# Kernel optimization log

Hardware: AMD Instinct MI355X
Metric: run time of the kernel (lower is better)

Reference implementation:

```python
import jax, jax.numpy as jnp
import numpy as np

NB_TS = 4          # module-level global nb_timestep in the original code
EMBED = 512
SQRT_DIM = float(np.sqrt(EMBED))


def _conv(x, w, b=None):
    # torch Conv2d(kernel=3, stride=1, padding=1), NCHW / OIHW
    y = jax.lax.conv_general_dilated(x, w, (1, 1), ((1, 1), (1, 1)),
                                     dimension_numbers=('NCHW', 'OIHW', 'NCHW'))
    if b is not None:
        y = y + b[None, :, None, None]
    return y


def setup_inputs() -> dict:
    B, C, H, W = 8, 512, 16, 16
    TXT = 256
    key = jax.random.key(0)
    ks = iter(jax.random.split(key, 40))

    def nrm(shape, s=0.02):
        return jax.random.normal(next(ks), shape, jnp.float32) * s

    inp = {
        'x':   jax.random.normal(next(ks), (B, C, H, W), jnp.float32),
        'txt': jax.random.normal(next(ks), (B, 1, TXT), jnp.float32),
        # attention convs
        'Wa_w': nrm((C, C, 3, 3)), 'Wa_b': nrm((C,)),
        'Ua_w': nrm((C, C, 3, 3)), 'Ua_b': nrm((C,)),
        'Va_w': nrm((1, C, 3, 3)),
        # gate convs
        'Wi_w': nrm((C, C, 3, 3)), 'Wi_b': nrm((C,)),
        'Ui_w': nrm((C, C, 3, 3)), 'Ui_b': nrm((C,)),
        'Wf_w': nrm((C, C, 3, 3)), 'Wf_b': nrm((C,)),
        'Uf_w': nrm((C, C, 3, 3)), 'Uf_b': nrm((C,)),
        'Wc_w': nrm((C, C, 3, 3)), 'Wc_b': nrm((C,)),
        'Uc_w': nrm((C, C, 3, 3)), 'Uc_b': nrm((C,)),
        'Wo_w': nrm((C, C, 3, 3)), 'Wo_b': nrm((C,)),
        'Uo_w': nrm((C, C, 3, 3)), 'Uo_b': nrm((C,)),
        # text attention linears (torch Linear weight layout [out, in])
        'WQ': nrm((EMBED * H * W, TXT)),
        'WK': nrm((EMBED, 1)),
        'WV': nrm((EMBED, 1)),
        'Wsum_w': nrm((1, EMBED)), 'Wsum_b': nrm((1,)),
    }
    return inp


def reference(x, txt, Wa_w, Wa_b, Ua_w, Ua_b, Va_w,
              Wi_w, Wi_b, Ui_w, Ui_b, Wf_w, Wf_b, Uf_w, Uf_b,
              Wc_w, Wc_b, Uc_w, Uc_b, Wo_w, Wo_b, Uo_w, Uo_b,
              WQ, WK, WV, Wsum_w, Wsum_b):
    B, _, Hs, Ws = x.shape
    txt2 = txt.reshape(txt.shape[0], txt.shape[2])  # [B, 256]
    h = x
    c = x
    # Q is timestep-invariant; hoist out of the loop (same math)
    Q = (txt2 @ WQ.T).reshape(B, Hs, Ws, EMBED)  # [B,H,W,E]
    for _ in range(NB_TS):
        Z = _conv(jnp.tanh(_conv(h, Wa_w, Wa_b) + _conv(x, Ua_w, Ua_b)), Va_w)  # [B,1,H,W]
        A1 = jax.nn.softmax(Z, axis=1)          # softmax over channel dim of size 1 (faithful)
        Ap = jnp.transpose(A1, (0, 2, 3, 1))    # [B,H,W,1]
        K = Ap @ WK.T                            # [B,H,W,E]
        V = Ap @ WV.T                            # [B,H,W,E]
        scores = jnp.sum(Q * K, axis=3, keepdims=True) / SQRT_DIM  # [B,H,W,1]
        attn = jax.nn.softmax(scores, axis=1)    # torch softmax(dim=1) -> over H axis
        # repeat(...,embed_dim)*V is just a broadcast multiply
        A2 = (attn * V) @ Wsum_w.T + Wsum_b      # [B,H,W,1]
        A2 = jnp.transpose(A2, (0, 3, 1, 2))     # [B,1,H,W]
        myA = A1 + A2
        AM = myA * x
        i = jax.nn.sigmoid(_conv(AM, Wi_w, Wi_b) + _conv(h, Ui_w, Ui_b))
        f = jax.nn.sigmoid(_conv(AM, Wf_w, Wf_b) + _conv(h, Uf_w, Uf_b))
        o = jax.nn.sigmoid(_conv(AM, Wo_w, Wo_b) + _conv(h, Uo_w, Uo_b))
        g = jnp.tanh(_conv(AM, Wc_w, Wc_b) + _conv(h, Uc_w, Uc_b))
        c = g * i + f * c
        h = jnp.tanh(c) * o
    return h
```

## Files before the change

### kernel.cpp

```cpp
#include <hip/hip_runtime.h>

typedef unsigned short u16;
typedef __attribute__((ext_vector_type(8))) _Float16 f16x8;
typedef __attribute__((ext_vector_type(4))) float f32x4;
typedef __attribute__((ext_vector_type(4))) int i32x4;
typedef __attribute__((ext_vector_type(4))) unsigned short us4;

__device__ __forceinline__ u16 f2h(float f) {
  _Float16 h = (_Float16)f;
  return __builtin_bit_cast(unsigned short, h);
}
__device__ __forceinline__ float sigm(float v) { return 1.0f / (1.0f + __expf(-v)); }
__device__ __forceinline__ float tanh_(float v) {
  float t = __expf(-2.0f * fabsf(v));
  float r = (1.0f - t) / (1.0f + t);
  return v >= 0.0f ? r : -r;
}

typedef const __attribute__((address_space(1))) unsigned int* gas_t;
typedef __attribute__((address_space(3))) unsigned int* las_t;
__device__ __forceinline__ void gl16(const u16* g, u16* l) {
  __builtin_amdgcn_global_load_lds((gas_t)g, (las_t)l, 16, 0, 0);
}

__global__ void prep_big(const float* __restrict__ WQ, const float* __restrict__ WK,
                         const float* __restrict__ txt, const float* __restrict__ WV,
                         const float* __restrict__ Wsw, const float* __restrict__ Wsb,
                         const float* __restrict__ wi, const float* __restrict__ wf,
                         const float* __restrict__ wo, const float* __restrict__ wc,
                         const float* __restrict__ ui, const float* __restrict__ uf,
                         const float* __restrict__ uo, const float* __restrict__ uc,
                         u16* __restrict__ dstW, u16* __restrict__ dstU,
                         float* __restrict__ scores, float* __restrict__ sb) {
  __shared__ float wk[512];
  __shared__ float red[4];
  int tid = threadIdx.x;
  if (blockIdx.x < 256) {
    int lane = tid & 63, wave = tid >> 6;
    wk[tid] = WK[tid];
    wk[tid + 256] = WK[tid + 256];
    __syncthreads();
    size_t p = blockIdx.x;
    const float* base = WQ + p * 131072 + tid;
    float m = 0.f;
#pragma unroll 8
    for (int e = 0; e < 512; ++e) m = fmaf(base[(size_t)e * 256], wk[e], m);
    for (int b = 0; b < 8; ++b) {
      float v = m * txt[b * 256 + tid];
#pragma unroll
      for (int off = 32; off > 0; off >>= 1) v += __shfl_down(v, off, 64);
      if (lane == 0) red[wave] = v;
      __syncthreads();
      if (tid == 0)
        scores[b * 256 + p] = (red[0] + red[1] + red[2] + red[3]) * 0.044194173824159216f;
      __syncthreads();
    }
    if (blockIdx.x == 0) {
      float v = WV[tid] * Wsw[tid] + WV[tid + 256] * Wsw[tid + 256];
#pragma unroll
      for (int off = 32; off > 0; off >>= 1) v += __shfl_down(v, off, 64);
      if (lane == 0) red[wave] = v;
      __syncthreads();
      if (tid == 0) {
        sb[0] = red[0] + red[1] + red[2] + red[3];
        sb[1] = Wsb[0];
      }
    }
    return;
  }
  int idx = (blockIdx.x - 256) * 256 + tid;
  const int PERSET = 4718592;
  int set = idx >= PERSET ? 1 : 0;
  int o = idx - set * PERSET;
  int j = o * 2;
  int ci = j & 31;
  int gch = (j >> 5) & 63;
  int t = j >> 11;
  int k9 = t % 9;
  int cc = t / 9;
  int chunk = cc & 15, chgrp = cc >> 4;
  int gate = gch >> 4, chrow = gch & 15;
  int ch = chgrp * 16 + chrow;
  int cin = chunk * 32 + ci;
  const float* s;
  if (set == 0) s = gate == 0 ? wi : gate == 1 ? wf : gate == 2 ? wo : wc;
  else          s = gate == 0 ? ui : gate == 1 ? uf : gate == 2 ? uo : uc;
  size_t si = (size_t)(ch * 512 + cin) * 9 + k9;
  unsigned int lo = f2h(s[si]);
  unsigned int hi = f2h(s[si + 9]);
  unsigned int* d = (unsigned int*)(set == 0 ? dstW : dstU);
  d[o] = lo | (hi << 16);
}

__global__ void prep_inputs(const float* __restrict__ x, const float* __restrict__ scores,
                            const float* __restrict__ sb,
                            u16* __restrict__ AM, u16* __restrict__ H0) {
  int idx = blockIdx.x * 256 + threadIdx.x;
  int ch = idx & 511, p = (idx >> 9) & 255, b = idx >> 17;
  int w = p & 15, h = p >> 4;
  float s = sb[0], b0 = sb[1];
  float mx = -1e30f;
#pragma unroll
  for (int hh = 0; hh < 16; ++hh) mx = fmaxf(mx, scores[b * 256 + hh * 16 + w]);
  float den = 0.f, my = 0.f;
#pragma unroll
  for (int hh = 0; hh < 16; ++hh) {
    float e = __expf(scores[b * 256 + hh * 16 + w] - mx);
    den += e;
    if (hh == h) my = e;
  }
  float coef = 1.0f + b0 + s * my / den;
  float xv = x[(size_t)(b * 512 + ch) * 256 + p];
  AM[idx] = f2h(coef * xv);
  H0[idx] = f2h(xv);
}

template <int MODE>
__launch_bounds__(256, 1)
__global__ void conv4(const u16* __restrict__ inA, const u16* __restrict__ inH,
                      const u16* __restrict__ wW, const u16* __restrict__ wU,
                      const float* __restrict__ bWi, const float* __restrict__ bUi,
                      const float* __restrict__ bWf, const float* __restrict__ bUf,
                      const float* __restrict__ bWo, const float* __restrict__ bUo,
                      const float* __restrict__ bWc, const float* __restrict__ bUc,
                      float* __restrict__ G, const float* __restrict__ c_src,
                      float* __restrict__ c_dst, u16* __restrict__ h_out,
                      float* __restrict__ out) {
  __shared__ __align__(16) u16 Alds[2][9 * 64 * 32];
  __shared__ __align__(16) u16 Blds[2][18 * 18 * 32];
  const int tid = threadIdx.x;
  const int b = blockIdx.x >> 5, chgrp = blockIdx.x & 31;
  const int wave = tid >> 6, lane = tid & 63;
  const int row = lane & 15, quad = lane >> 4;
  const int NCH = (MODE == 0) ? 32 : 16;

  {
    i32x4 z = {0, 0, 0, 0};
    i32x4* bz = (i32x4*)Blds;
#pragma unroll
    for (int i = 0; i < 11; ++i) {
      int k = tid + 256 * i;
      if (k < 2592) bz[k] = z;
    }
  }

  const u16* wsrcW = (MODE == 0) ? wW + (size_t)chgrp * 294912 : nullptr;
  const u16* wsrcU = wU + (size_t)chgrp * 294912;
  const u16* isrcA = (MODE == 0) ? inA + (size_t)b * 131072 : nullptr;
  const u16* isrcH = inH + (size_t)b * 131072;

  auto stage = [&](int k, int buf) {
    const u16* gw;
    const u16* gi;
    if (MODE == 0 && k < 16) { gw = wsrcW + k * 18432; gi = isrcA + (k & 15) * 32; }
    else                     { gw = wsrcU + (k & 15) * 18432; gi = isrcH + (k & 15) * 32; }
#pragma unroll
    for (int i = 0; i < 9; ++i)
      gl16(gw + (size_t)(i * 256 + tid) * 8, &Alds[buf][(i * 256 + (tid & 192)) * 8]);
#pragma unroll
    for (int j = 0; j < 4; ++j) {
      int y = j * 4 + wave;
      gl16(gi + (size_t)(y * 16 + (lane >> 2)) * 512 + (lane & 3) * 8,
           &Blds[buf][(y + 1) * 576 + 32]);
    }
  };

  f32x4 acc[4][4];
#pragma unroll
  for (int m = 0; m < 4; ++m)
#pragma unroll
    for (int n = 0; n < 4; ++n) acc[m][n] = (f32x4){0.f, 0.f, 0.f, 0.f};

  const int ch0 = chgrp * 16 + quad * 4;
  float* gptr = G + (((size_t)blockIdx.x * 4 + wave) * 16) * 256 + lane * 4;

  stage(0, 0);
  __syncthreads();

#pragma unroll 2
  for (int k = 0; k < NCH; ++k) {
    int cur = k & 1;
    if (k + 1 < NCH) stage(k + 1, cur ^ 1);
    const u16* A = Alds[cur];
    const u16* B = Blds[cur];
#pragma unroll
    for (int kx = 0; kx < 3; ++kx) {
      f16x8 bfr[6];
#pragma unroll
      for (int jj = 0; jj < 6; ++jj)
        bfr[jj] = *(const f16x8*)(&B[(wave * 4 + jj) * 576 + (row + kx) * 32 + quad * 8]);
#pragma unroll
      for (int ky = 0; ky < 3; ++ky) {
#pragma unroll
        for (int m = 0; m < 4; ++m) {
          f16x8 af = *(const f16x8*)(&A[((ky * 3 + kx) * 64 + m * 16 + row) * 32 + quad * 8]);
#pragma unroll
          for (int n = 0; n < 4; ++n)
            acc[m][n] = __builtin_amdgcn_mfma_f32_16x16x32_f16(af, bfr[n + ky], acc[m][n], 0, 0, 0);
        }
      }
    }
    if constexpr (MODE == 0) {
      if (k == 15) {
#pragma unroll
        for (int m = 0; m < 4; ++m) {
          const float* bw = m == 0 ? bWi : m == 1 ? bWf : m == 2 ? bWo : bWc;
          const float* bu = m == 0 ? bUi : m == 1 ? bUf : m == 2 ? bUo : bUc;
          f32x4 bias;
#pragma unroll
          for (int r = 0; r < 4; ++r) bias[r] = bw[ch0 + r] + bu[ch0 + r];
#pragma unroll
          for (int n = 0; n < 4; ++n) {
            acc[m][n] = acc[m][n] + bias;
            *(f32x4*)(gptr + (m * 4 + n) * 256) = acc[m][n];
          }
        }
      }
    }
    __syncthreads();
  }

#pragma unroll
  for (int n = 0; n < 4; ++n) {
    const int p = (wave * 4 + n) * 16 + row;
    f32x4 zi = acc[0][n], zf = acc[1][n], zo = acc[2][n], zg = acc[3][n];
    if constexpr (MODE != 0) {
      zi = zi + *(const f32x4*)(gptr + (0 + n) * 256);
      zf = zf + *(const f32x4*)(gptr + (4 + n) * 256);
      zo = zo + *(const f32x4*)(gptr + (8 + n) * 256);
      zg = zg + *(const f32x4*)(gptr + (12 + n) * 256);
    }
    f32x4 cold;
#pragma unroll
    for (int r = 0; r < 4; ++r)
      cold[r] = c_src[(size_t)(b * 512 + ch0 + r) * 256 + p];
    f32x4 cnew, hv;
#pragma unroll
    for (int r = 0; r < 4; ++r) {
      float iv = sigm(zi[r]);
      float fv = sigm(zf[r]);
      float ov = sigm(zo[r]);
      float gv = tanh_(zg[r]);
      float cn = fmaf(gv, iv, fv * cold[r]);
      cnew[r] = cn;
      hv[r] = tanh_(cn) * ov;
    }
    if constexpr (MODE != 2) {
#pragma unroll
      for (int r = 0; r < 4; ++r)
        c_dst[(size_t)(b * 512 + ch0 + r) * 256 + p] = cnew[r];
      us4 hb;
      hb[0] = f2h(hv[0]); hb[1] = f2h(hv[1]);
      hb[2] = f2h(hv[2]); hb[3] = f2h(hv[3]);
      *(us4*)(h_out + (size_t)b * 131072 + (size_t)p * 512 + ch0) = hb;
    } else {
#pragma unroll
      for (int r = 0; r < 4; ++r)
        out[(size_t)(b * 512 + ch0 + r) * 256 + p] = hv[r];
    }
  }
}

extern "C" void kernel_launch(void* const* d_in, const int* in_sizes, int n_in,
                              void* d_out, int out_size, void* d_ws, size_t ws_size,
                              hipStream_t stream) {
  const float* x    = (const float*)d_in[0];
  const float* txt  = (const float*)d_in[1];
  const float* Wi_w = (const float*)d_in[7];
  const float* Wi_b = (const float*)d_in[8];
  const float* Ui_w = (const float*)d_in[9];
  const float* Ui_b = (const float*)d_in[10];
  const float* Wf_w = (const float*)d_in[11];
  const float* Wf_b = (const float*)d_in[12];
  const float* Uf_w = (const float*)d_in[13];
  const float* Uf_b = (const float*)d_in[14];
  const float* Wc_w = (const float*)d_in[15];
  const float* Wc_b = (const float*)d_in[16];
  const float* Uc_w = (const float*)d_in[17];
  const float* Uc_b = (const float*)d_in[18];
  const float* Wo_w = (const float*)d_in[19];
  const float* Wo_b = (const float*)d_in[20];
  const float* Uo_w = (const float*)d_in[21];
  const float* Uo_b = (const float*)d_in[22];
  const float* WQ   = (const float*)d_in[23];
  const float* WK   = (const float*)d_in[24];
  const float* WV   = (const float*)d_in[25];
  const float* Wsw  = (const float*)d_in[26];
  const float* Wsb  = (const float*)d_in[27];
  (void)in_sizes; (void)n_in; (void)ws_size;

  char* ws = (char*)d_ws;
  size_t off = 0;
  auto carve = [&](size_t n) {
    char* p = ws + off;
    off += (n + 255) & ~(size_t)255;
    return p;
  };
  u16* WswzW    = (u16*)carve(18874368);
  u16* WswzU    = (u16*)carve(18874368);
  u16* AM       = (u16*)carve(2097152);
  u16* H0       = (u16*)carve(2097152);
  u16* H1       = (u16*)carve(2097152);
  float* G      = (float*)carve(16777216);
  float* C      = (float*)carve(4194304);
  float* scores = (float*)carve(8192);
  float* sb     = (float*)carve(256);

  prep_big<<<37120, 256, 0, stream>>>(WQ, WK, txt, WV, Wsw, Wsb,
                                      Wi_w, Wf_w, Wo_w, Wc_w,
                                      Ui_w, Uf_w, Uo_w, Uc_w,
                                      WswzW, WswzU, scores, sb);
  prep_inputs<<<4096, 256, 0, stream>>>(x, scores, sb, AM, H0);

  conv4<0><<<256, 256, 0, stream>>>(AM, H0, WswzW, WswzU,
                                    Wi_b, Ui_b, Wf_b, Uf_b, Wo_b, Uo_b, Wc_b, Uc_b,
                                    G, x, C, H1, nullptr);
  conv4<1><<<256, 256, 0, stream>>>(nullptr, H1, nullptr, WswzU,
                                    nullptr, nullptr, nullptr, nullptr,
                                    nullptr, nullptr, nullptr, nullptr,
                                    G, C, C, H0, nullptr);
  conv4<1><<<256, 256, 0, stream>>>(nullptr, H0, nullptr, WswzU,
                                    nullptr, nullptr, nullptr, nullptr,
                                    nullptr, nullptr, nullptr, nullptr,
                                    G, C, C, H1, nullptr);
  conv4<2><<<256, 256, 0, stream>>>(nullptr, H1, nullptr, WswzU,
                                    nullptr, nullptr, nullptr, nullptr,
                                    nullptr, nullptr, nullptr, nullptr,
                                    G, C, nullptr, nullptr, (float*)d_out);
}
```

Measured before the change: 555.8 us.

## Split conv blocks by spatial half, single-buffer LDS, restructure prep kernels

The score GEMV is split over 8 embedding slices, with partial results combined by atomicAdd into a zeroed buffer. The weight swizzle now stages each strip through LDS and writes it out with coalesced 16-byte stores. The conv kernels split each batch image into two row halves, which doubles the grid to 512 blocks and allows 2 blocks per CU. In exchange they drop LDS double buffering and use explicit sync-stage-sync, so loads no longer overlap compute within a block. Weights are also loaded twice as often in total, since each half refetches them.

```diff
diff --git a/kernel.cpp b/kernel.cpp
--- a/kernel.cpp
+++ b/kernel.cpp
@@ -32,33 +32,35 @@
                          const float* __restrict__ uo, const float* __restrict__ uc,
                          u16* __restrict__ dstW, u16* __restrict__ dstU,
                          float* __restrict__ scores, float* __restrict__ sb) {
-  __shared__ float wk[512];
+  __shared__ __align__(16) u16 L[9 * 64 * 32];
+  __shared__ float wk[64];
   __shared__ float red[4];
   int tid = threadIdx.x;
-  if (blockIdx.x < 256) {
-    int lane = tid & 63, wave = tid >> 6;
-    wk[tid] = WK[tid];
-    wk[tid + 256] = WK[tid + 256];
+  if (blockIdx.x < 2048) {
+    int p = blockIdx.x & 255;
+    int es = blockIdx.x >> 8;
+    if (tid < 64) wk[tid] = WK[es * 64 + tid];
     __syncthreads();
-    size_t p = blockIdx.x;
-    const float* base = WQ + p * 131072 + tid;
+    const float* base = WQ + (size_t)p * 131072 + (size_t)es * 16384 + tid;
     float m = 0.f;
 #pragma unroll 8
-    for (int e = 0; e < 512; ++e) m = fmaf(base[(size_t)e * 256], wk[e], m);
+    for (int e = 0; e < 64; ++e) m = fmaf(base[(size_t)e * 256], wk[e], m);
+    int lane = tid & 63, wave = tid >> 6;
     for (int b = 0; b < 8; ++b) {
       float v = m * txt[b * 256 + tid];
 #pragma unroll
-      for (int off = 32; off > 0; off >>= 1) v += __shfl_down(v, off, 64);
+      for (int off = 32; off; off >>= 1) v += __shfl_down(v, off, 64);
       if (lane == 0) red[wave] = v;
       __syncthreads();
       if (tid == 0)
-        scores[b * 256 + p] = (red[0] + red[1] + red[2] + red[3]) * 0.044194173824159216f;
+        atomicAdd(&scores[b * 256 + p],
+                  (red[0] + red[1] + red[2] + red[3]) * 0.044194173824159216f);
       __syncthreads();
     }
     if (blockIdx.x == 0) {
       float v = WV[tid] * Wsw[tid] + WV[tid + 256] * Wsw[tid + 256];
 #pragma unroll
-      for (int off = 32; off > 0; off >>= 1) v += __shfl_down(v, off, 64);
+      for (int off = 32; off; off >>= 1) v += __shfl_down(v, off, 64);
       if (lane == 0) red[wave] = v;
       __syncthreads();
       if (tid == 0) {
@@ -68,28 +70,30 @@
     }
     return;
   }
-  int idx = (blockIdx.x - 256) * 256 + tid;
-  const int PERSET = 4718592;
-  int set = idx >= PERSET ? 1 : 0;
-  int o = idx - set * PERSET;
-  int j = o * 2;
-  int ci = j & 31;
-  int gch = (j >> 5) & 63;
-  int t = j >> 11;
-  int k9 = t % 9;
-  int cc = t / 9;
-  int chunk = cc & 15, chgrp = cc >> 4;
+  int sbid = blockIdx.x - 2048;
+  int set = sbid >> 9;
+  int chgrp = (sbid >> 4) & 31;
+  int chunk = sbid & 15;
+  int q = tid & 3, gch = tid >> 2;
   int gate = gch >> 4, chrow = gch & 15;
   int ch = chgrp * 16 + chrow;
-  int cin = chunk * 32 + ci;
   const float* s;
   if (set == 0) s = gate == 0 ? wi : gate == 1 ? wf : gate == 2 ? wo : wc;
   else          s = gate == 0 ? ui : gate == 1 ? uf : gate == 2 ? uo : uc;
-  size_t si = (size_t)(ch * 512 + cin) * 9 + k9;
-  unsigned int lo = f2h(s[si]);
-  unsigned int hi = f2h(s[si + 9]);
-  unsigned int* d = (unsigned int*)(set == 0 ? dstW : dstU);
-  d[o] = lo | (hi << 16);
+  const float* strip = s + (size_t)(ch * 512 + chunk * 32) * 9;
+#pragma unroll
+  for (int c8 = 0; c8 < 8; ++c8) {
+    int cl = q * 8 + c8;
+#pragma unroll
+    for (int k9 = 0; k9 < 9; ++k9)
+      L[(k9 * 64 + gch) * 32 + cl] = f2h(strip[cl * 9 + k9]);
+  }
+  __syncthreads();
+  u16* dst = (set == 0 ? dstW : dstU) + (size_t)(chgrp * 16 + chunk) * 18432;
+  i32x4* d4 = (i32x4*)dst;
+  i32x4* l4 = (i32x4*)L;
+#pragma unroll
+  for (int i = 0; i < 9; ++i) d4[i * 256 + tid] = l4[i * 256 + tid];
 }
 
 __global__ void prep_inputs(const float* __restrict__ x, const float* __restrict__ scores,
@@ -116,7 +120,7 @@
 }
 
 template <int MODE>
-__launch_bounds__(256, 1)
+__launch_bounds__(256, 2)
 __global__ void conv4(const u16* __restrict__ inA, const u16* __restrict__ inH,
                       const u16* __restrict__ wW, const u16* __restrict__ wU,
                       const float* __restrict__ bWi, const float* __restrict__ bUi,
@@ -126,76 +130,78 @@
                       float* __restrict__ G, const float* __restrict__ c_src,
                       float* __restrict__ c_dst, u16* __restrict__ h_out,
                       float* __restrict__ out) {
-  __shared__ __align__(16) u16 Alds[2][9 * 64 * 32];
-  __shared__ __align__(16) u16 Blds[2][18 * 18 * 32];
+  __shared__ __align__(16) u16 Alds[9 * 64 * 32];
+  __shared__ __align__(16) u16 Blds[10 * 18 * 32];
   const int tid = threadIdx.x;
-  const int b = blockIdx.x >> 5, chgrp = blockIdx.x & 31;
+  const int chgrp = blockIdx.x & 31;
+  const int nhalf = (blockIdx.x >> 5) & 1;
+  const int b = blockIdx.x >> 6;
   const int wave = tid >> 6, lane = tid & 63;
   const int row = lane & 15, quad = lane >> 4;
   const int NCH = (MODE == 0) ? 32 : 16;
+  const int gyBase = nhalf * 8 - 1;
 
   {
     i32x4 z = {0, 0, 0, 0};
     i32x4* bz = (i32x4*)Blds;
 #pragma unroll
-    for (int i = 0; i < 11; ++i) {
+    for (int i = 0; i < 6; ++i) {
       int k = tid + 256 * i;
-      if (k < 2592) bz[k] = z;
-    }
-  }
-
-  const u16* wsrcW = (MODE == 0) ? wW + (size_t)chgrp * 294912 : nullptr;
+      if (k < 1440) bz[k] = z;
+    }
+  }
+  __syncthreads();
+
+  const u16* wsrcW = wW + (size_t)chgrp * 294912;
   const u16* wsrcU = wU + (size_t)chgrp * 294912;
-  const u16* isrcA = (MODE == 0) ? inA + (size_t)b * 131072 : nullptr;
+  const u16* isrcA = inA + (size_t)b * 131072;
   const u16* isrcH = inH + (size_t)b * 131072;
 
-  auto stage = [&](int k, int buf) {
+  auto stage = [&](int k) {
     const u16* gw;
     const u16* gi;
-    if (MODE == 0 && k < 16) { gw = wsrcW + k * 18432; gi = isrcA + (k & 15) * 32; }
+    if (MODE == 0 && k < 16) { gw = wsrcW + k * 18432; gi = isrcA + k * 32; }
     else                     { gw = wsrcU + (k & 15) * 18432; gi = isrcH + (k & 15) * 32; }
 #pragma unroll
     for (int i = 0; i < 9; ++i)
-      gl16(gw + (size_t)(i * 256 + tid) * 8, &Alds[buf][(i * 256 + (tid & 192)) * 8]);
-#pragma unroll
-    for (int j = 0; j < 4; ++j) {
-      int y = j * 4 + wave;
-      gl16(gi + (size_t)(y * 16 + (lane >> 2)) * 512 + (lane & 3) * 8,
-           &Blds[buf][(y + 1) * 576 + 32]);
+      gl16(gw + (i * 256 + tid) * 8, &Alds[(i * 256 + wave * 64) * 8]);
+#pragma unroll
+    for (int j = 0; j < 3; ++j) {
+      int r = j * 4 + wave;
+      int gy = gyBase + r;
+      if (r < 10 && gy >= 0 && gy < 16)
+        gl16(gi + (size_t)(gy * 16 + (lane >> 2)) * 512 + (lane & 3) * 8,
+             &Blds[r * 576 + 32]);
     }
   };
 
-  f32x4 acc[4][4];
+  f32x4 acc[4][2];
 #pragma unroll
   for (int m = 0; m < 4; ++m)
 #pragma unroll
-    for (int n = 0; n < 4; ++n) acc[m][n] = (f32x4){0.f, 0.f, 0.f, 0.f};
+    for (int n = 0; n < 2; ++n) acc[m][n] = (f32x4){0.f, 0.f, 0.f, 0.f};
 
   const int ch0 = chgrp * 16 + quad * 4;
-  float* gptr = G + (((size_t)blockIdx.x * 4 + wave) * 16) * 256 + lane * 4;
-
-  stage(0, 0);
+  float* gptr = G + (size_t)blockIdx.x * 8192 + wave * 2048 + lane * 4;
+
+  stage(0);
   __syncthreads();
 
-#pragma unroll 2
+#pragma unroll 1
   for (int k = 0; k < NCH; ++k) {
-    int cur = k & 1;
-    if (k + 1 < NCH) stage(k + 1, cur ^ 1);
-    const u16* A = Alds[cur];
-    const u16* B = Blds[cur];
 #pragma unroll
     for (int kx = 0; kx < 3; ++kx) {
-      f16x8 bfr[6];
-#pragma unroll
-      for (int jj = 0; jj < 6; ++jj)
-        bfr[jj] = *(const f16x8*)(&B[(wave * 4 + jj) * 576 + (row + kx) * 32 + quad * 8]);
+      f16x8 bfr[4];
+#pragma unroll
+      for (int jj = 0; jj < 4; ++jj)
+        bfr[jj] = *(const f16x8*)(&Blds[(wave * 2 + jj) * 576 + (row + kx) * 32 + quad * 8]);
 #pragma unroll
       for (int ky = 0; ky < 3; ++ky) {
 #pragma unroll
         for (int m = 0; m < 4; ++m) {
-          f16x8 af = *(const f16x8*)(&A[((ky * 3 + kx) * 64 + m * 16 + row) * 32 + quad * 8]);
-#pragma unroll
-          for (int n = 0; n < 4; ++n)
+          f16x8 af = *(const f16x8*)(&Alds[((ky * 3 + kx) * 64 + m * 16 + row) * 32 + quad * 8]);
+#pragma unroll
+          for (int n = 0; n < 2; ++n)
             acc[m][n] = __builtin_amdgcn_mfma_f32_16x16x32_f16(af, bfr[n + ky], acc[m][n], 0, 0, 0);
         }
       }
@@ -210,25 +216,29 @@
 #pragma unroll
           for (int r = 0; r < 4; ++r) bias[r] = bw[ch0 + r] + bu[ch0 + r];
 #pragma unroll
-          for (int n = 0; n < 4; ++n) {
+          for (int n = 0; n < 2; ++n) {
             acc[m][n] = acc[m][n] + bias;
-            *(f32x4*)(gptr + (m * 4 + n) * 256) = acc[m][n];
+            *(f32x4*)(gptr + (m * 2 + n) * 256) = acc[m][n];
           }
         }
       }
     }
-    __syncthreads();
-  }
-
-#pragma unroll
-  for (int n = 0; n < 4; ++n) {
-    const int p = (wave * 4 + n) * 16 + row;
+    if (k + 1 < NCH) {
+      __syncthreads();
+      stage(k + 1);
+      __syncthreads();
+    }
+  }
+
+#pragma unroll
+  for (int n = 0; n < 2; ++n) {
+    const int p = (nhalf * 8 + wave * 2 + n) * 16 + row;
     f32x4 zi = acc[0][n], zf = acc[1][n], zo = acc[2][n], zg = acc[3][n];
     if constexpr (MODE != 0) {
       zi = zi + *(const f32x4*)(gptr + (0 + n) * 256);
-      zf = zf + *(const f32x4*)(gptr + (4 + n) * 256);
-      zo = zo + *(const f32x4*)(gptr + (8 + n) * 256);
-      zg = zg + *(const f32x4*)(gptr + (12 + n) * 256);
+      zf = zf + *(const f32x4*)(gptr + (2 + n) * 256);
+      zo = zo + *(const f32x4*)(gptr + (4 + n) * 256);
+      zg = zg + *(const f32x4*)(gptr + (6 + n) * 256);
     }
     f32x4 cold;
 #pragma unroll
@@ -306,24 +316,26 @@
   float* scores = (float*)carve(8192);
   float* sb     = (float*)carve(256);
 
-  prep_big<<<37120, 256, 0, stream>>>(WQ, WK, txt, WV, Wsw, Wsb,
-                                      Wi_w, Wf_w, Wo_w, Wc_w,
-                                      Ui_w, Uf_w, Uo_w, Uc_w,
-                                      WswzW, WswzU, scores, sb);
+  hipMemsetAsync(scores, 0, 8192, stream);
+
+  prep_big<<<3072, 256, 0, stream>>>(WQ, WK, txt, WV, Wsw, Wsb,
+                                     Wi_w, Wf_w, Wo_w, Wc_w,
+                                     Ui_w, Uf_w, Uo_w, Uc_w,
+                                     WswzW, WswzU, scores, sb);
   prep_inputs<<<4096, 256, 0, stream>>>(x, scores, sb, AM, H0);
 
-  conv4<0><<<256, 256, 0, stream>>>(AM, H0, WswzW, WswzU,
+  conv4<0><<<512, 256, 0, stream>>>(AM, H0, WswzW, WswzU,
                                     Wi_b, Ui_b, Wf_b, Uf_b, Wo_b, Uo_b, Wc_b, Uc_b,
                                     G, x, C, H1, nullptr);
-  conv4<1><<<256, 256, 0, stream>>>(nullptr, H1, nullptr, WswzU,
+  conv4<1><<<512, 256, 0, stream>>>(nullptr, H1, nullptr, WswzU,
                                     nullptr, nullptr, nullptr, nullptr,
                                     nullptr, nullptr, nullptr, nullptr,
                                     G, C, C, H0, nullptr);
-  conv4<1><<<256, 256, 0, stream>>>(nullptr, H0, nullptr, WswzU,
+  conv4<1><<<512, 256, 0, stream>>>(nullptr, H0, nullptr, WswzU,
                                     nullptr, nullptr, nullptr, nullptr,
                                     nullptr, nullptr, nullptr, nullptr,
                                     G, C, C, H1, nullptr);
-  conv4<2><<<256, 256, 0, stream>>>(nullptr, H1, nullptr, WswzU,
+  conv4<2><<<512, 256, 0, stream>>>(nullptr, H1, nullptr, WswzU,
                                     nullptr, nullptr, nullptr, nullptr,
                                     nullptr, nullptr, nullptr, nullptr,
                                     G, C, nullptr, nullptr, (float*)d_out);
```

Result: faster. 525.4 us (-5.5%).
